# Optimization experiments

Hardware: AMD Instinct MI355X
Metric: run time of the kernel (lower is better)

The kernel has to match this reference:

```python
import jax, jax.numpy as jnp
import numpy as np

IM_SIZE = 512
NUM_PIXELS = IM_SIZE * IM_SIZE  # 262144 = 2**18, power of two for FWHT
COMPRESSION_RATIO = 0.25
BATCH, CHANNELS = 16, 3


def fwht(x):
    """Orthonormal fast Walsh-Hadamard transform along the last axis.

    x: [..., N] with N a power of two. Iterative butterfly: log2(N) stages,
    each pairing elements at stride h within blocks of size 2h.
    """
    orig_shape = x.shape
    N = orig_shape[-1]
    x = x.reshape(-1, N)
    h = 1
    while h < N:
        # [rows, N] -> [rows, N/(2h), 2, h]; axis 2 indexes the two butterfly halves
        x = x.reshape(-1, N // (2 * h), 2, h)
        a = x[:, :, 0, :]
        b = x[:, :, 1, :]
        x = jnp.stack((a + b, a - b), axis=2).reshape(-1, N)
        h *= 2
    scale = jnp.asarray(1.0 / np.sqrt(N), dtype=x.dtype)  # orthonormal scaling
    return (x * scale).reshape(orig_shape)


def setup_inputs() -> dict:
    key = jax.random.key(0)
    k_x, k_perm = jax.random.split(key)
    x = jax.random.normal(k_x, (BATCH, CHANNELS, IM_SIZE, IM_SIZE), dtype=jnp.float32)
    # Binary sampling mask: n_select random pattern indices set to 1 (sampling_method='random')
    n_select = max(1, int(round(NUM_PIXELS * COMPRESSION_RATIO)))
    perm = jax.random.permutation(k_perm, NUM_PIXELS)
    mask = jnp.zeros((NUM_PIXELS,), dtype=jnp.float32).at[perm[:n_select]].set(1.0)
    return {"x": x, "mask": mask}


def reference(x, mask):
    """SPCModel.forward_pass: FWHT over flattened image + diagonal mask multiply."""
    B, C, H, W = x.shape
    x_flat = x.reshape(B, C, H * W)            # [B, C, N]
    measurements = fwht(x_flat)                 # [B, C, N]
    return measurements * mask[None, None, :]   # diagonal operator M
```

## Files before the change

kernel.cpp:

```cpp
#include <hip/hip_runtime.h>


constexpr int IM = 512;
constexpr int NPIX = IM * IM;
constexpr int NIMG = 48;

__device__ __forceinline__ void bf3(float f[8]) {
#define BF(i, j) { float a_ = f[i]; float b_ = f[j]; f[i] = a_ + b_; f[j] = a_ - b_; }
  BF(0, 1); BF(2, 3); BF(4, 5); BF(6, 7);
  BF(0, 2); BF(1, 3); BF(4, 6); BF(5, 7);
  BF(0, 4); BF(1, 5); BF(2, 6); BF(3, 7);
#undef BF
}

__global__ __launch_bounds__(256) void fwht_rows(const float* __restrict__ in,
                                                 float* __restrict__ out) {
  const int wave = threadIdx.x >> 6;
  const int l = threadIdx.x & 63;
  const size_t row = (size_t)blockIdx.x * 4 + wave;
  const float* p = in + row * IM + l * 8;

  float4 A  = *reinterpret_cast<const float4*>(p);
  float4 Bv = *reinterpret_cast<const float4*>(p + 4);
  float f[8] = {A.x, A.y, A.z, A.w, Bv.x, Bv.y, Bv.z, Bv.w};

  bf3(f);

#pragma unroll
  for (int s = 0; s < 6; ++s) {
    const int m = 1 << s;
    const float sgn = (l & m) ? -1.0f : 1.0f;
#pragma unroll
    for (int j = 0; j < 8; ++j) {
      float t = __shfl_xor(f[j], m, 64);
      f[j] = fmaf(f[j], sgn, t);
    }
  }

  float* q = out + row * IM + l * 8;
  *reinterpret_cast<float4*>(q)     = make_float4(f[0], f[1], f[2], f[3]);
  *reinterpret_cast<float4*>(q + 4) = make_float4(f[4], f[5], f[6], f[7]);
}

__global__ __launch_bounds__(256) void fwht_cols(float* __restrict__ buf,
                                                 const float* __restrict__ mask) {
  __shared__ float tile[IM * 32];

  const int img = blockIdx.y;
  const int c0 = blockIdx.x * 32;
  const size_t base = (size_t)img * NPIX;
  const int t = threadIdx.x;
  const int c = t & 31;
  const int a0 = t >> 5;

#pragma unroll 4
  for (int i = 0; i < 64; ++i) {
    const int a = a0 + 8 * i;
    tile[a * 32 + (c ^ (a & 31))] = buf[base + (size_t)a * IM + c0 + c];
  }
  __syncthreads();

  const int l = t & 63;
  const int w = t >> 6;

  float v[8][8];
#pragma unroll
  for (int k = 0; k < 8; ++k) {
    const int a = l + 64 * k;
#pragma unroll
    for (int cc = 0; cc < 8; ++cc)
      v[k][cc] = tile[a * 32 + ((8 * w + cc) ^ (a & 31))];
  }

#pragma unroll
  for (int s = 0; s < 6; ++s) {
    const int m = 1 << s;
    const float sgn = (l & m) ? -1.0f : 1.0f;
#pragma unroll
    for (int k = 0; k < 8; ++k)
#pragma unroll
      for (int cc = 0; cc < 8; ++cc) {
        float tt = __shfl_xor(v[k][cc], m, 64);
        v[k][cc] = fmaf(v[k][cc], sgn, tt);
      }
  }

#pragma unroll
  for (int cc = 0; cc < 8; ++cc) {
    float g[8];
#pragma unroll
    for (int k = 0; k < 8; ++k) g[k] = v[k][cc];
    bf3(g);
#pragma unroll
    for (int k = 0; k < 8; ++k) v[k][cc] = g[k];
  }
  __syncthreads();

#pragma unroll
  for (int k = 0; k < 8; ++k) {
    const int a = l + 64 * k;
#pragma unroll
    for (int cc = 0; cc < 8; ++cc)
      tile[a * 32 + ((8 * w + cc) ^ (a & 31))] = v[k][cc];
  }
  __syncthreads();

#pragma unroll 4
  for (int i = 0; i < 64; ++i) {
    const int a = a0 + 8 * i;
    const int pix = a * IM + c0 + c;
    buf[base + pix] = tile[a * 32 + (c ^ (a & 31))] * mask[pix] * (1.0f / 512.0f);
  }
}

extern "C" void kernel_launch(void* const* d_in, const int* in_sizes, int n_in,
                              void* d_out, int out_size, void* d_ws, size_t ws_size,
                              hipStream_t stream) {
  (void)in_sizes; (void)n_in; (void)d_ws; (void)ws_size; (void)out_size;
  const float* x    = (const float*)d_in[0];
  const float* mask = (const float*)d_in[1];
  float* out = (float*)d_out;

  fwht_rows<<<dim3(NIMG * IM / 4), dim3(256), 0, stream>>>(x, out);
  fwht_cols<<<dim3(IM / 32, NIMG), dim3(256), 0, stream>>>(out, mask);
}
```

Measured before the change: 135.4 us.

## Restructure 2D FWHT into shared-memory radix-8 pass and register column pass

```diff
diff --git a/kernel.cpp b/kernel.cpp
--- a/kernel.cpp
+++ b/kernel.cpp
@@ -13,103 +13,107 @@
 #undef BF
 }
 
-__global__ __launch_bounds__(256) void fwht_rows(const float* __restrict__ in,
-                                                 float* __restrict__ out) {
-  const int wave = threadIdx.x >> 6;
-  const int l = threadIdx.x & 63;
-  const size_t row = (size_t)blockIdx.x * 4 + wave;
-  const float* p = in + row * IM + l * 8;
+__device__ __forceinline__ int sw(int a, int b, int c) {
+  return (c << 6) + ((((b << 3) + a)) ^ (c << 2));
+}
 
-  float4 A  = *reinterpret_cast<const float4*>(p);
-  float4 Bv = *reinterpret_cast<const float4*>(p + 4);
-  float f[8] = {A.x, A.y, A.z, A.w, Bv.x, Bv.y, Bv.z, Bv.w};
+__global__ __launch_bounds__(512) void fwht_pass1(const float* __restrict__ in,
+                                                  float* __restrict__ out) {
+  __shared__ float tile[8 * 512];
+  const int img = blockIdx.y;
+  const int r0  = blockIdx.x;
+  const size_t base = (size_t)img * NPIX;
+  const int t = threadIdx.x;
+  const int k = t >> 6;
 
-  bf3(f);
+  {
+    const int o = t & 63;
+    const float* p = in + base + (size_t)(r0 + 64 * k) * IM + o * 8;
+    float4 A = *(const float4*)p, B = *(const float4*)(p + 4);
+    float f[8] = {A.x, A.y, A.z, A.w, B.x, B.y, B.z, B.w};
+    bf3(f);
+    const int b = o & 7, c = o >> 3;
+    float* tp = &tile[k * 512];
+    const int base0 = sw(0, b, c);
+    *(float4*)&tp[base0]     = make_float4(f[0], f[1], f[2], f[3]);
+    *(float4*)&tp[base0 ^ 4] = make_float4(f[4], f[5], f[6], f[7]);
+  }
+  __syncthreads();
+
+  {
+    const int a = t & 7, c = (t >> 3) & 7;
+    float* tp = &tile[k * 512];
+    float g[8];
+#pragma unroll
+    for (int b = 0; b < 8; ++b) g[b] = tp[sw(a, b, c)];
+    bf3(g);
+#pragma unroll
+    for (int b = 0; b < 8; ++b) tp[sw(a, b, c)] = g[b];
+  }
+  __syncthreads();
+
+  {
+    const int a = t & 7, b = (t >> 3) & 7;
+    float* tp = &tile[k * 512];
+    float g[8];
+#pragma unroll
+    for (int c = 0; c < 8; ++c) g[c] = tp[sw(a, b, c)];
+    bf3(g);
+#pragma unroll
+    for (int c = 0; c < 8; ++c) tp[sw(a, b, c)] = g[c];
+  }
+  __syncthreads();
+
+  {
+    const int j = t;
+    const int off = sw(j & 7, (j >> 3) & 7, j >> 6);
+    float g[8];
+#pragma unroll
+    for (int kk = 0; kk < 8; ++kk) g[kk] = tile[kk * 512 + off];
+    bf3(g);
+#pragma unroll
+    for (int kk = 0; kk < 8; ++kk)
+      out[base + (size_t)(r0 + 64 * kk) * IM + j] = g[kk];
+  }
+}
+
+__global__ __launch_bounds__(256) void fwht_pass2(float* __restrict__ buf,
+                                                  const float* __restrict__ mask) {
+  __shared__ float tile[64 * 256];
+  const int img = blockIdx.z;
+  const int R0 = blockIdx.y * 64;
+  const int C0 = blockIdx.x * 256;
+  const size_t base = (size_t)img * NPIX;
+  const int t = threadIdx.x;
+
+  {
+    const int q  = (t & 63) * 4;
+    const int rw = t >> 6;
+#pragma unroll
+    for (int i = 0; i < 16; ++i) {
+      const int r = rw + 4 * i;
+      float4 v = *(const float4*)&buf[base + (size_t)(R0 + r) * IM + C0 + q];
+      *(float4*)&tile[r * 256 + q] = v;
+    }
+  }
+  __syncthreads();
+
+  float v[64];
+#pragma unroll
+  for (int r = 0; r < 64; ++r) v[r] = tile[r * 256 + t];
 
 #pragma unroll
   for (int s = 0; s < 6; ++s) {
     const int m = 1 << s;
-    const float sgn = (l & m) ? -1.0f : 1.0f;
 #pragma unroll
-    for (int j = 0; j < 8; ++j) {
-      float t = __shfl_xor(f[j], m, 64);
-      f[j] = fmaf(f[j], sgn, t);
-    }
-  }
-
-  float* q = out + row * IM + l * 8;
-  *reinterpret_cast<float4*>(q)     = make_float4(f[0], f[1], f[2], f[3]);
-  *reinterpret_cast<float4*>(q + 4) = make_float4(f[4], f[5], f[6], f[7]);
-}
-
-__global__ __launch_bounds__(256) void fwht_cols(float* __restrict__ buf,
-                                                 const float* __restrict__ mask) {
-  __shared__ float tile[IM * 32];
-
-  const int img = blockIdx.y;
-  const int c0 = blockIdx.x * 32;
-  const size_t base = (size_t)img * NPIX;
-  const int t = threadIdx.x;
-  const int c = t & 31;
-  const int a0 = t >> 5;
-
-#pragma unroll 4
-  for (int i = 0; i < 64; ++i) {
-    const int a = a0 + 8 * i;
-    tile[a * 32 + (c ^ (a & 31))] = buf[base + (size_t)a * IM + c0 + c];
-  }
-  __syncthreads();
-
-  const int l = t & 63;
-  const int w = t >> 6;
-
-  float v[8][8];
-#pragma unroll
-  for (int k = 0; k < 8; ++k) {
-    const int a = l + 64 * k;
-#pragma unroll
-    for (int cc = 0; cc < 8; ++cc)
-      v[k][cc] = tile[a * 32 + ((8 * w + cc) ^ (a & 31))];
+    for (int r = 0; r < 64; ++r)
+      if (!(r & m)) { float x = v[r], y = v[r | m]; v[r] = x + y; v[r | m] = x - y; }
   }
 
 #pragma unroll
-  for (int s = 0; s < 6; ++s) {
-    const int m = 1 << s;
-    const float sgn = (l & m) ? -1.0f : 1.0f;
-#pragma unroll
-    for (int k = 0; k < 8; ++k)
-#pragma unroll
-      for (int cc = 0; cc < 8; ++cc) {
-        float tt = __shfl_xor(v[k][cc], m, 64);
-        v[k][cc] = fmaf(v[k][cc], sgn, tt);
-      }
-  }
-
-#pragma unroll
-  for (int cc = 0; cc < 8; ++cc) {
-    float g[8];
-#pragma unroll
-    for (int k = 0; k < 8; ++k) g[k] = v[k][cc];
-    bf3(g);
-#pragma unroll
-    for (int k = 0; k < 8; ++k) v[k][cc] = g[k];
-  }
-  __syncthreads();
-
-#pragma unroll
-  for (int k = 0; k < 8; ++k) {
-    const int a = l + 64 * k;
-#pragma unroll
-    for (int cc = 0; cc < 8; ++cc)
-      tile[a * 32 + ((8 * w + cc) ^ (a & 31))] = v[k][cc];
-  }
-  __syncthreads();
-
-#pragma unroll 4
-  for (int i = 0; i < 64; ++i) {
-    const int a = a0 + 8 * i;
-    const int pix = a * IM + c0 + c;
-    buf[base + pix] = tile[a * 32 + (c ^ (a & 31))] * mask[pix] * (1.0f / 512.0f);
+  for (int r = 0; r < 64; ++r) {
+    const int pix = (R0 + r) * IM + C0 + t;
+    buf[base + pix] = v[r] * mask[pix] * (1.0f / 512.0f);
   }
 }
 
@@ -121,6 +125,6 @@
   const float* mask = (const float*)d_in[1];
   float* out = (float*)d_out;
 
-  fwht_rows<<<dim3(NIMG * IM / 4), dim3(256), 0, stream>>>(x, out);
-  fwht_cols<<<dim3(IM / 32, NIMG), dim3(256), 0, stream>>>(out, mask);
+  fwht_pass1<<<dim3(64, NIMG), dim3(512), 0, stream>>>(x, out);
+  fwht_pass2<<<dim3(2, 8, NIMG), dim3(256), 0, stream>>>(out, mask);
 }
```

New measurement: 120.1 us. 1.13x faster.
